# Performance work log

Measured on AMD Instinct MI355X. Metric: run time of the kernel, lower is better.

Reference implementation:

```python
import jax, jax.numpy as jnp
import numpy as np

B, F0, D = 4096, 39, 16
CROSS_LAYER_SIZE = (128, 128)


def _he_uniform(key, shape):
    fan_in = int(np.prod(shape[:-1]))
    limit = np.sqrt(6.0 / fan_in)
    return jax.random.uniform(key, shape, jnp.float32, -limit, limit)


def setup_inputs() -> dict:
    key = jax.random.key(0)
    k_x, k_f0, k_f1, k_w, k_b = jax.random.split(key, 5)
    x = jax.random.normal(k_x, (B, F0, D), dtype=jnp.float32)
    # field_nums with direct=False: [39, 128//2=64, 64]
    f0 = _he_uniform(k_f0, (F0 * F0, CROSS_LAYER_SIZE[0]))          # (1521, 128)
    f1 = _he_uniform(k_f1, (F0 * (CROSS_LAYER_SIZE[0] // 2), CROSS_LAYER_SIZE[1]))  # (2496, 128)
    out_dim = CROSS_LAYER_SIZE[0] // 2 + CROSS_LAYER_SIZE[1]        # 192
    dense_w = _he_uniform(k_w, (out_dim, 1))
    dense_b = jnp.zeros((1,), dtype=jnp.float32)
    return {"x": x, "f0": f0, "f1": f1, "dense_w": dense_w, "dense_b": dense_b}


def reference(x, f0, f1, dense_w, dense_b):
    # CIN forward (direct=False, use_bias=False, use_residual=False, relu)
    # x: (B, F0, D)
    filters = [f0, f1]
    n_layers = len(CROSS_LAYER_SIZE)
    h = x  # hidden state, (B, Fk, D)
    finals = []
    for idx, L in enumerate(CROSS_LAYER_SIZE):
        Fk = h.shape[1]
        # filter f_ has shape (F0*Fk, L) with i (field of x0) major, j (field of h) minor
        Wr = filters[idx].reshape(F0, Fk, L)
        # fused outer product + conv1d (kernel width 1 == matmul over i,j):
        # z[b, m, d] = sum_{i,j} x[b,i,d] * h[b,j,d] * W[i,j,m]
        z = jnp.einsum('bid,bjd,ijm->bmd', x, h, Wr)  # (B, L, D)
        z = jax.nn.relu(z)
        if idx != n_layers - 1:
            # split along feature-map axis: first half feeds next layer,
            # second half goes to output
            h = z[:, : L // 2, :]
            finals.append(z[:, L // 2:, :])
        else:
            finals.append(z)
    result = jnp.sum(jnp.concatenate(finals, axis=1), axis=-1)  # (B, 192)
    return result @ dense_w + dense_b  # (B, 1)
```

## Files before the change

### kernel.cpp

```cpp
#include <hip/hip_runtime.h>


typedef _Float16 h2    __attribute__((ext_vector_type(2)));
typedef _Float16 f16x8 __attribute__((ext_vector_type(8)));
typedef __attribute__((ext_vector_type(16))) float f32x16;

__global__ __launch_bounds__(256)
void CIN_repack(const float* __restrict__ f0, const float* __restrict__ f1,
                uint4* __restrict__ ws)
{
    const int tid  = blockIdx.x * 256 + threadIdx.x;
    const int n    = tid & 127;
    const int slot = tid >> 7;
    const int half = slot & 1;
    const int kh   = (slot >> 1) & 1;
    const int ch   = slot >> 2;
    float v[8];
    if (ch < 50) {
        const int ig = ch / 5, jg = ch - ig * 5;
        const int i = ig * 4 + kh * 2 + half;
        const bool iok = (i < 39);
#pragma unroll
        for (int t = 0; t < 8; ++t) {
            const int j = jg * 8 + t;
            v[t] = (iok && j < 39) ? f0[(i * 39 + j) * 128 + n] : 0.f;
        }
    } else {
        const int c1 = ch - 50;
        const int jg = c1 / 5, ig = c1 - jg * 5;
        const int j = jg * 4 + kh * 2 + half;
#pragma unroll
        for (int t = 0; t < 8; ++t) {
            const int i = ig * 8 + t;
            v[t] = (i < 39) ? f1[(i * 64 + j) * 128 + n] : 0.f;
        }
    }
    union { h2 h[4]; uint4 q; } pk;
#pragma unroll
    for (int t = 0; t < 4; ++t)
        pk.h[t] = h2{(_Float16)v[2 * t], (_Float16)v[2 * t + 1]};
    const int lane = half * 32 + (n & 31);
    const int cg   = n >> 5;
    ws[ch * 512 + kh * 256 + cg * 64 + lane] = pk.q;
}

__global__ __launch_bounds__(256, 2)
void CIN_main(const float* __restrict__ x,
              const char* __restrict__ wsB,
              const float* __restrict__ dw,
              const float* __restrict__ db,
              float* __restrict__ out)
{
    __shared__ __align__(16) _Float16 xsH[8][16][64];
    __shared__ __align__(4)  _Float16 hsH[8][64][18];
    __shared__ float dws[192];
    __shared__ float red[2][2][4];

    const int tid  = threadIdx.x;
    const int w    = tid >> 6;
    const int lane = tid & 63;
    const int g    = w & 1;
    const int hh   = w >> 1;
    const int half = lane >> 5;
    const int d    = lane & 15;
    const int bsel = (lane >> 4) & 1;
    const int g4   = g * 4;

    const char* wbase = wsB + lane * 16 + hh * 2048 + 2560;
    f16x8 Bb[2][2][2];
    auto loadBg = [&](int ch, f16x8 (&B)[2][2]) {
        const char* p0 = wbase + (size_t)ch * 8192;
        B[0][0] = *(const f16x8*)(p0 - 2560);
        B[0][1] = *(const f16x8*)(p0 - 1536);
        B[1][0] = *(const f16x8*)(p0 + 1536);
        B[1][1] = *(const f16x8*)(p0 + 2560);
    };

    loadBg(0, Bb[0]);
    loadBg(1, Bb[1]);

    const float4* xg4 = (const float4*)(x + (size_t)blockIdx.x * 8 * 624);
    for (int e4 = tid; e4 < 1248; e4 += 256) {
        float4 v = xg4[e4];
        int bb = e4 / 156, r = e4 - bb * 156;
        int i = r >> 2, d0 = (r & 3) * 4;
        xsH[bb][d0 + 0][i] = (_Float16)v.x; xsH[bb][d0 + 1][i] = (_Float16)v.y;
        xsH[bb][d0 + 2][i] = (_Float16)v.z; xsH[bb][d0 + 3][i] = (_Float16)v.w;
    }
    if (tid < 128) { int bb = tid >> 4, dd = tid & 15; xsH[bb][dd][39] = (_Float16)0.f; }
    if (tid < 192) dws[tid] = dw[tid];
    __syncthreads();

    h2 xv[2][20];
#pragma unroll
    for (int p = 0; p < 2; ++p) {
        const uint4* src = (const uint4*)&xsH[g4 + p * 2 + bsel][d][0];
#pragma unroll
        for (int q5 = 0; q5 < 5; ++q5) {
            union { uint4 q; h2 h[4]; } u;
            u.q = src[q5];
#pragma unroll
            for (int t = 0; t < 4; ++t) xv[p][q5 * 4 + t] = u.h[t];
        }
    }

    f32x16 acc[2][2];
#pragma unroll
    for (int p = 0; p < 2; ++p)
#pragma unroll
        for (int c = 0; c < 2; ++c)
#pragma unroll
            for (int r = 0; r < 16; ++r) acc[p][c][r] = 0.f;

    h2 xiv2[2][2];

#pragma unroll 1
    for (int o = 0; o < 5; ++o) {
#pragma unroll
        for (int u = 0; u < 10; ++u) {
            const int ch = o * 10 + u;
            const int jg = u % 5;
            if (jg == 0) {
                const int ib = (o * 2 + u / 5) * 4;
#pragma unroll
                for (int p = 0; p < 2; ++p)
#pragma unroll
                    for (int kh = 0; kh < 2; ++kh) {
                        _Float16 s = xsH[g4 + p * 2 + bsel][d][ib + kh * 2 + half];
                        xiv2[p][kh] = h2{s, s};
                    }
            }
            f16x8 A[2][2];
#pragma unroll
            for (int p = 0; p < 2; ++p)
#pragma unroll
                for (int kh = 0; kh < 2; ++kh) {
                    union { h2 h[4]; f16x8 v; } a;
#pragma unroll
                    for (int q = 0; q < 4; ++q)
                        a.h[q] = xiv2[p][kh] * xv[p][jg * 4 + q];
                    A[p][kh] = a.v;
                }
#pragma unroll
            for (int p = 0; p < 2; ++p)
#pragma unroll
                for (int c = 0; c < 2; ++c) {
                    acc[p][c] = __builtin_amdgcn_mfma_f32_32x32x16_f16(A[p][0], Bb[u & 1][0][c], acc[p][c], 0, 0, 0);
                    acc[p][c] = __builtin_amdgcn_mfma_f32_32x32x16_f16(A[p][1], Bb[u & 1][1][c], acc[p][c], 0, 0, 0);
                }
            loadBg(ch + 2, Bb[u & 1]);
        }
    }

    float cs[4] = {0.f, 0.f, 0.f, 0.f};
    if (hh == 0) {
#pragma unroll
        for (int p = 0; p < 2; ++p)
#pragma unroll
            for (int c = 0; c < 2; ++c)
#pragma unroll
                for (int r = 0; r < 16; r += 2) {
                    const int row = (r & 3) + 8 * (r >> 2) + 4 * half;
                    h2 pr = h2{(_Float16)fmaxf(acc[p][c][r],     0.f),
                               (_Float16)fmaxf(acc[p][c][r + 1], 0.f)};
                    *(h2*)&hsH[g4 + p * 2 + (row >> 4)][c * 32 + (lane & 31)][row & 15] = pr;
                }
    } else {
#pragma unroll
        for (int p = 0; p < 2; ++p)
#pragma unroll
            for (int c = 0; c < 2; ++c) {
                const float dwv = dws[c * 32 + (lane & 31)];
#pragma unroll
                for (int r = 0; r < 16; ++r) {
                    const int row = (r & 3) + 8 * (r >> 2) + 4 * half;
                    cs[p * 2 + (row >> 4)] += fmaxf(acc[p][c][r], 0.f) * dwv;
                }
            }
    }
#pragma unroll
    for (int p = 0; p < 2; ++p)
#pragma unroll
        for (int c = 0; c < 2; ++c)
#pragma unroll
            for (int r = 0; r < 16; ++r) acc[p][c][r] = 0.f;
    __syncthreads();

#pragma unroll 1
    for (int o2 = 0; o2 < 8; ++o2) {
#pragma unroll
        for (int u = 0; u < 10; ++u) {
            const int ch = 50 + o2 * 10 + u;
            const int ig2 = u % 5;
            if (ig2 == 0) {
                const int jb = (o2 * 2 + u / 5) * 4;
#pragma unroll
                for (int p = 0; p < 2; ++p)
#pragma unroll
                    for (int kh = 0; kh < 2; ++kh) {
                        _Float16 s = hsH[g4 + p * 2 + bsel][jb + kh * 2 + half][d];
                        xiv2[p][kh] = h2{s, s};
                    }
            }
            f16x8 A[2][2];
#pragma unroll
            for (int p = 0; p < 2; ++p)
#pragma unroll
                for (int kh = 0; kh < 2; ++kh) {
                    union { h2 h[4]; f16x8 v; } a;
#pragma unroll
                    for (int q = 0; q < 4; ++q)
                        a.h[q] = xiv2[p][kh] * xv[p][ig2 * 4 + q];
                    A[p][kh] = a.v;
                }
#pragma unroll
            for (int p = 0; p < 2; ++p)
#pragma unroll
                for (int c = 0; c < 2; ++c) {
                    acc[p][c] = __builtin_amdgcn_mfma_f32_32x32x16_f16(A[p][0], Bb[u & 1][0][c], acc[p][c], 0, 0, 0);
                    acc[p][c] = __builtin_amdgcn_mfma_f32_32x32x16_f16(A[p][1], Bb[u & 1][1][c], acc[p][c], 0, 0, 0);
                }
            int chn = ch + 2; if (chn > 129) chn = 129;
            loadBg(chn, Bb[u & 1]);
        }
    }

#pragma unroll
    for (int p = 0; p < 2; ++p)
#pragma unroll
        for (int c = 0; c < 2; ++c) {
            const float dwv = dws[64 + (2 * hh + c) * 32 + (lane & 31)];
#pragma unroll
            for (int r = 0; r < 16; ++r) {
                const int row = (r & 3) + 8 * (r >> 2) + 4 * half;
                cs[p * 2 + (row >> 4)] += fmaxf(acc[p][c][r], 0.f) * dwv;
            }
        }
#pragma unroll
    for (int rr = 0; rr < 4; ++rr)
#pragma unroll
        for (int off = 32; off > 0; off >>= 1)
            cs[rr] += __shfl_xor(cs[rr], off, 64);
    if (lane == 0) {
#pragma unroll
        for (int rr = 0; rr < 4; ++rr) red[g][hh][rr] = cs[rr];
    }
    __syncthreads();
    if (tid < 8) {
        const int g2 = tid >> 2, rr = tid & 3;
        out[blockIdx.x * 8 + g2 * 4 + rr] = red[g2][0][rr] + red[g2][1][rr] + db[0];
    }
}

extern "C" void kernel_launch(void* const* d_in, const int* in_sizes, int n_in,
                              void* d_out, int out_size, void* d_ws, size_t ws_size,
                              hipStream_t stream)
{
    const float* x  = (const float*)d_in[0];
    const float* f0 = (const float*)d_in[1];
    const float* f1 = (const float*)d_in[2];
    const float* dw = (const float*)d_in[3];
    const float* db = (const float*)d_in[4];
    float* out = (float*)d_out;

    CIN_repack<<<dim3(260), dim3(256), 0, stream>>>(f0, f1, (uint4*)d_ws);
    CIN_main<<<dim3(512), dim3(256), 0, stream>>>(x, (const char*)d_ws, dw, db, out);
}
```

Measured before the change: 131.3 us.

## Split CIN work across waves by output column and pad x smem rows

Each wave now owns one 32-wide output-column slice for all 8 batch rows, instead of splitting batch rows into two groups and columns into two halves. Each wave therefore loads only its own weight slice, halving per-wave B-fragment global loads and B registers, while building A fragments for 4 row-pairs. The x shared-memory tile is repacked with a padded row stride of 72 halves and a padded per-batch stride to reduce bank conflicts. The cost is more VALU work per wave to form the A products and more x registers, which may raise register pressure.

```diff
diff --git a/kernel.cpp b/kernel.cpp
--- a/kernel.cpp
+++ b/kernel.cpp
@@ -4,6 +4,8 @@
 typedef _Float16 h2    __attribute__((ext_vector_type(2)));
 typedef _Float16 f16x8 __attribute__((ext_vector_type(8)));
 typedef __attribute__((ext_vector_type(16))) float f32x16;
+
+#define XBB 1160
 
 __global__ __launch_bounds__(256)
 void CIN_repack(const float* __restrict__ f0, const float* __restrict__ f1,
@@ -51,29 +53,25 @@
               const float* __restrict__ db,
               float* __restrict__ out)
 {
-    __shared__ __align__(16) _Float16 xsH[8][16][64];
+    __shared__ __align__(16) _Float16 xsH[8 * XBB];
     __shared__ __align__(4)  _Float16 hsH[8][64][18];
     __shared__ float dws[192];
-    __shared__ float red[2][2][4];
+    __shared__ float red[4][8];
 
     const int tid  = threadIdx.x;
     const int w    = tid >> 6;
     const int lane = tid & 63;
-    const int g    = w & 1;
-    const int hh   = w >> 1;
     const int half = lane >> 5;
     const int d    = lane & 15;
     const int bsel = (lane >> 4) & 1;
-    const int g4   = g * 4;
-
-    const char* wbase = wsB + lane * 16 + hh * 2048 + 2560;
-    f16x8 Bb[2][2][2];
-    auto loadBg = [&](int ch, f16x8 (&B)[2][2]) {
+    const int col  = lane & 31;
+
+    const char* wbase = wsB + lane * 16 + w * 1024 + 2048;
+    f16x8 Bb[2][2];
+    auto loadBg = [&](int ch, f16x8 (&B)[2]) {
         const char* p0 = wbase + (size_t)ch * 8192;
-        B[0][0] = *(const f16x8*)(p0 - 2560);
-        B[0][1] = *(const f16x8*)(p0 - 1536);
-        B[1][0] = *(const f16x8*)(p0 + 1536);
-        B[1][1] = *(const f16x8*)(p0 + 2560);
+        B[0] = *(const f16x8*)(p0 - 2048);
+        B[1] = *(const f16x8*)(p0 + 2048);
     };
 
     loadBg(0, Bb[0]);
@@ -84,17 +82,18 @@
         float4 v = xg4[e4];
         int bb = e4 / 156, r = e4 - bb * 156;
         int i = r >> 2, d0 = (r & 3) * 4;
-        xsH[bb][d0 + 0][i] = (_Float16)v.x; xsH[bb][d0 + 1][i] = (_Float16)v.y;
-        xsH[bb][d0 + 2][i] = (_Float16)v.z; xsH[bb][d0 + 3][i] = (_Float16)v.w;
-    }
-    if (tid < 128) { int bb = tid >> 4, dd = tid & 15; xsH[bb][dd][39] = (_Float16)0.f; }
+        _Float16* bp = xsH + bb * XBB + i;
+        bp[(d0 + 0) * 72] = (_Float16)v.x; bp[(d0 + 1) * 72] = (_Float16)v.y;
+        bp[(d0 + 2) * 72] = (_Float16)v.z; bp[(d0 + 3) * 72] = (_Float16)v.w;
+    }
+    if (tid < 128) { int bb = tid >> 4, dd = tid & 15; xsH[bb * XBB + dd * 72 + 39] = (_Float16)0.f; }
     if (tid < 192) dws[tid] = dw[tid];
     __syncthreads();
 
-    h2 xv[2][20];
-#pragma unroll
-    for (int p = 0; p < 2; ++p) {
-        const uint4* src = (const uint4*)&xsH[g4 + p * 2 + bsel][d][0];
+    h2 xv[4][20];
+#pragma unroll
+    for (int p = 0; p < 4; ++p) {
+        const uint4* src = (const uint4*)(xsH + (p * 2 + bsel) * XBB + d * 72);
 #pragma unroll
         for (int q5 = 0; q5 < 5; ++q5) {
             union { uint4 q; h2 h[4]; } u;
@@ -104,15 +103,13 @@
         }
     }
 
-    f32x16 acc[2][2];
-#pragma unroll
-    for (int p = 0; p < 2; ++p)
-#pragma unroll
-        for (int c = 0; c < 2; ++c)
-#pragma unroll
-            for (int r = 0; r < 16; ++r) acc[p][c][r] = 0.f;
-
-    h2 xiv2[2][2];
+    f32x16 acc[4];
+#pragma unroll
+    for (int p = 0; p < 4; ++p)
+#pragma unroll
+        for (int r = 0; r < 16; ++r) acc[p][r] = 0.f;
+
+    h2 xiv2[4][2];
 
 #pragma unroll 1
     for (int o = 0; o < 5; ++o) {
@@ -123,67 +120,53 @@
             if (jg == 0) {
                 const int ib = (o * 2 + u / 5) * 4;
 #pragma unroll
-                for (int p = 0; p < 2; ++p)
+                for (int p = 0; p < 4; ++p)
 #pragma unroll
                     for (int kh = 0; kh < 2; ++kh) {
-                        _Float16 s = xsH[g4 + p * 2 + bsel][d][ib + kh * 2 + half];
+                        _Float16 s = xsH[(p * 2 + bsel) * XBB + d * 72 + ib + kh * 2 + half];
                         xiv2[p][kh] = h2{s, s};
                     }
             }
-            f16x8 A[2][2];
-#pragma unroll
-            for (int p = 0; p < 2; ++p)
-#pragma unroll
-                for (int kh = 0; kh < 2; ++kh) {
-                    union { h2 h[4]; f16x8 v; } a;
-#pragma unroll
-                    for (int q = 0; q < 4; ++q)
-                        a.h[q] = xiv2[p][kh] * xv[p][jg * 4 + q];
-                    A[p][kh] = a.v;
+#pragma unroll
+            for (int p = 0; p < 4; ++p) {
+                union { h2 h[4]; f16x8 v; } a0, a1;
+#pragma unroll
+                for (int q = 0; q < 4; ++q) {
+                    a0.h[q] = xiv2[p][0] * xv[p][jg * 4 + q];
+                    a1.h[q] = xiv2[p][1] * xv[p][jg * 4 + q];
                 }
-#pragma unroll
-            for (int p = 0; p < 2; ++p)
-#pragma unroll
-                for (int c = 0; c < 2; ++c) {
-                    acc[p][c] = __builtin_amdgcn_mfma_f32_32x32x16_f16(A[p][0], Bb[u & 1][0][c], acc[p][c], 0, 0, 0);
-                    acc[p][c] = __builtin_amdgcn_mfma_f32_32x32x16_f16(A[p][1], Bb[u & 1][1][c], acc[p][c], 0, 0, 0);
-                }
+                acc[p] = __builtin_amdgcn_mfma_f32_32x32x16_f16(a0.v, Bb[u & 1][0], acc[p], 0, 0, 0);
+                acc[p] = __builtin_amdgcn_mfma_f32_32x32x16_f16(a1.v, Bb[u & 1][1], acc[p], 0, 0, 0);
+            }
             loadBg(ch + 2, Bb[u & 1]);
         }
     }
 
-    float cs[4] = {0.f, 0.f, 0.f, 0.f};
-    if (hh == 0) {
-#pragma unroll
-        for (int p = 0; p < 2; ++p)
-#pragma unroll
-            for (int c = 0; c < 2; ++c)
-#pragma unroll
-                for (int r = 0; r < 16; r += 2) {
-                    const int row = (r & 3) + 8 * (r >> 2) + 4 * half;
-                    h2 pr = h2{(_Float16)fmaxf(acc[p][c][r],     0.f),
-                               (_Float16)fmaxf(acc[p][c][r + 1], 0.f)};
-                    *(h2*)&hsH[g4 + p * 2 + (row >> 4)][c * 32 + (lane & 31)][row & 15] = pr;
-                }
+    float cs[8] = {0.f, 0.f, 0.f, 0.f, 0.f, 0.f, 0.f, 0.f};
+    if (w < 2) {
+#pragma unroll
+        for (int p = 0; p < 4; ++p)
+#pragma unroll
+            for (int r = 0; r < 16; r += 2) {
+                const int row = (r & 3) + 8 * (r >> 2) + 4 * half;
+                h2 pr = h2{(_Float16)fmaxf(acc[p][r],     0.f),
+                           (_Float16)fmaxf(acc[p][r + 1], 0.f)};
+                *(h2*)&hsH[p * 2 + (row >> 4)][w * 32 + col][row & 15] = pr;
+            }
     } else {
-#pragma unroll
-        for (int p = 0; p < 2; ++p)
-#pragma unroll
-            for (int c = 0; c < 2; ++c) {
-                const float dwv = dws[c * 32 + (lane & 31)];
-#pragma unroll
-                for (int r = 0; r < 16; ++r) {
-                    const int row = (r & 3) + 8 * (r >> 2) + 4 * half;
-                    cs[p * 2 + (row >> 4)] += fmaxf(acc[p][c][r], 0.f) * dwv;
-                }
-            }
-    }
-#pragma unroll
-    for (int p = 0; p < 2; ++p)
-#pragma unroll
-        for (int c = 0; c < 2; ++c)
-#pragma unroll
-            for (int r = 0; r < 16; ++r) acc[p][c][r] = 0.f;
+        const float dwv = dws[(w - 2) * 32 + col];
+#pragma unroll
+        for (int p = 0; p < 4; ++p)
+#pragma unroll
+            for (int r = 0; r < 16; ++r) {
+                const int row = (r & 3) + 8 * (r >> 2) + 4 * half;
+                cs[p * 2 + (row >> 4)] += fmaxf(acc[p][r], 0.f) * dwv;
+            }
+    }
+#pragma unroll
+    for (int p = 0; p < 4; ++p)
+#pragma unroll
+        for (int r = 0; r < 16; ++r) acc[p][r] = 0.f;
     __syncthreads();
 
 #pragma unroll 1
@@ -195,61 +178,51 @@
             if (ig2 == 0) {
                 const int jb = (o2 * 2 + u / 5) * 4;
 #pragma unroll
-                for (int p = 0; p < 2; ++p)
+                for (int p = 0; p < 4; ++p)
 #pragma unroll
                     for (int kh = 0; kh < 2; ++kh) {
-                        _Float16 s = hsH[g4 + p * 2 + bsel][jb + kh * 2 + half][d];
+                        _Float16 s = hsH[p * 2 + bsel][jb + kh * 2 + half][d];
                         xiv2[p][kh] = h2{s, s};
                     }
             }
-            f16x8 A[2][2];
-#pragma unroll
-            for (int p = 0; p < 2; ++p)
-#pragma unroll
-                for (int kh = 0; kh < 2; ++kh) {
-                    union { h2 h[4]; f16x8 v; } a;
-#pragma unroll
-                    for (int q = 0; q < 4; ++q)
-                        a.h[q] = xiv2[p][kh] * xv[p][ig2 * 4 + q];
-                    A[p][kh] = a.v;
+#pragma unroll
+            for (int p = 0; p < 4; ++p) {
+                union { h2 h[4]; f16x8 v; } a0, a1;
+#pragma unroll
+                for (int q = 0; q < 4; ++q) {
+                    a0.h[q] = xiv2[p][0] * xv[p][ig2 * 4 + q];
+                    a1.h[q] = xiv2[p][1] * xv[p][ig2 * 4 + q];
                 }
-#pragma unroll
-            for (int p = 0; p < 2; ++p)
-#pragma unroll
-                for (int c = 0; c < 2; ++c) {
-                    acc[p][c] = __builtin_amdgcn_mfma_f32_32x32x16_f16(A[p][0], Bb[u & 1][0][c], acc[p][c], 0, 0, 0);
-                    acc[p][c] = __builtin_amdgcn_mfma_f32_32x32x16_f16(A[p][1], Bb[u & 1][1][c], acc[p][c], 0, 0, 0);
-                }
+                acc[p] = __builtin_amdgcn_mfma_f32_32x32x16_f16(a0.v, Bb[u & 1][0], acc[p], 0, 0, 0);
+                acc[p] = __builtin_amdgcn_mfma_f32_32x32x16_f16(a1.v, Bb[u & 1][1], acc[p], 0, 0, 0);
+            }
             int chn = ch + 2; if (chn > 129) chn = 129;
             loadBg(chn, Bb[u & 1]);
         }
     }
 
-#pragma unroll
-    for (int p = 0; p < 2; ++p)
-#pragma unroll
-        for (int c = 0; c < 2; ++c) {
-            const float dwv = dws[64 + (2 * hh + c) * 32 + (lane & 31)];
+    {
+        const float dwv = dws[64 + w * 32 + col];
+#pragma unroll
+        for (int p = 0; p < 4; ++p)
 #pragma unroll
             for (int r = 0; r < 16; ++r) {
                 const int row = (r & 3) + 8 * (r >> 2) + 4 * half;
-                cs[p * 2 + (row >> 4)] += fmaxf(acc[p][c][r], 0.f) * dwv;
-            }
-        }
-#pragma unroll
-    for (int rr = 0; rr < 4; ++rr)
+                cs[p * 2 + (row >> 4)] += fmaxf(acc[p][r], 0.f) * dwv;
+            }
+    }
+#pragma unroll
+    for (int rr = 0; rr < 8; ++rr)
 #pragma unroll
         for (int off = 32; off > 0; off >>= 1)
             cs[rr] += __shfl_xor(cs[rr], off, 64);
     if (lane == 0) {
 #pragma unroll
-        for (int rr = 0; rr < 4; ++rr) red[g][hh][rr] = cs[rr];
+        for (int rr = 0; rr < 8; ++rr) red[w][rr] = cs[rr];
     }
     __syncthreads();
-    if (tid < 8) {
-        const int g2 = tid >> 2, rr = tid & 3;
-        out[blockIdx.x * 8 + g2 * 4 + rr] = red[g2][0][rr] + red[g2][1][rr] + db[0];
-    }
+    if (tid < 8)
+        out[blockIdx.x * 8 + tid] = red[0][tid] + red[1][tid] + red[2][tid] + red[3][tid] + db[0];
 }
 
 extern "C" void kernel_launch(void* const* d_in, const int* in_sizes, int n_in,
```

Result: faster. 125.1 us (-4.7%).
